# Optimization experiments

Hardware: AMD Instinct MI355X
Metric: run time of the kernel (lower is better)

## Reference

```python
import jax, jax.numpy as jnp
import numpy as np

B, L, C, H, W, R = 2, 16, 64, 64, 128, 32
MH = 32          # forcing MLP hidden
M1, M2 = 8, 8    # spectral conv modes


def _conv2d(x, w, b):
    # x: (N, C, H, W), w: (O, C, kh, kw), SAME padding
    y = jax.lax.conv_general_dilated(x, w, (1, 1), 'SAME',
                                     dimension_numbers=('NCHW', 'OIHW', 'NCHW'))
    return y + b[None, :, None, None]


def setup_inputs():
    k = jax.random.split(jax.random.key(0), 24)
    r_min, r_max = 0.8, 0.99
    u1 = jax.random.uniform(k[0], (C, R))
    u2 = jax.random.uniform(k[1], (C, R))
    nu_log = jnp.log(-0.5 * jnp.log(u1 * (r_max ** 2 - r_min ** 2) + r_min ** 2))
    theta_log = jnp.log(u2 * (2.0 * np.pi))
    s = np.float32(1.0 / np.sqrt(C))
    rn = lambda kk, sh, sc=1.0: np.float32(sc) * jax.random.normal(kk, sh, jnp.float32)
    return {
        'x': rn(k[2], (B, L, C, H, W)),
        'nu_log': nu_log.astype(jnp.float32),
        'theta_log': theta_log.astype(jnp.float32),
        'mlp_w1': rn(k[3], (C, MH), 0.02), 'mlp_b1': jnp.zeros((MH,), jnp.float32),
        'mlp_w2': rn(k[4], (MH, C * R * 2), 0.02), 'mlp_b2': jnp.zeros((C * R * 2,), jnp.float32),
        'forcing_scale': jnp.asarray(0.1, jnp.float32),
        'U_r': rn(k[5], (C, H, R), 1.0 / np.sqrt(H)), 'U_i': rn(k[6], (C, H, R), 1.0 / np.sqrt(H)),
        'V_r': rn(k[7], (C, W, R), 1.0 / np.sqrt(W)), 'V_i': rn(k[8], (C, W, R), 1.0 / np.sqrt(W)),
        'projW_r': rn(k[9], (C, C), s), 'projW_i': rn(k[10], (C, C), s),
        'projb_r': jnp.zeros((C,), jnp.float32), 'projb_i': jnp.zeros((C,), jnp.float32),
        'swr1': rn(k[11], (C, C, M1, M2), s), 'swi1': rn(k[12], (C, C, M1, M2), s),
        'swr2': rn(k[13], (C, C, M1, M2), s), 'swi2': rn(k[14], (C, C, M1, M2), s),
        'convr_w': rn(k[15], (C, C, 3, 3), 0.05), 'convr_b': jnp.zeros((C,), jnp.float32),
        'convi_w': rn(k[16], (C, C, 3, 3), 0.05), 'convi_b': jnp.zeros((C,), jnp.float32),
        'fuse_w': rn(k[17], (C, 2 * C), s), 'fuse_b': jnp.zeros((C,), jnp.float32),
        'gate_w': rn(k[18], (C, C), s), 'gate_b': jnp.zeros((C,), jnp.float32),
        'ln_w': jnp.ones((H, W), jnp.float32), 'ln_b': jnp.zeros((H, W), jnp.float32),
    }


def reference(x, nu_log, theta_log, mlp_w1, mlp_b1, mlp_w2, mlp_b2, forcing_scale,
              U_r, U_i, V_r, V_i, projW_r, projW_i, projb_r, projb_i,
              swr1, swi1, swr2, swi2, convr_w, convr_b, convi_w, convi_b,
              fuse_w, fuse_b, gate_w, gate_b, ln_w, ln_b):
    b_, l_, c_, h_, w_ = x.shape
    # --- selective forcing: spatial-mean context modulates LRU poles ---
    ctx = x.mean((-2, -1))                                       # (B,L,C)
    hmid = jnp.tanh(ctx @ mlp_w1 + mlp_b1)
    delta = (hmid @ mlp_w2 + mlp_b2).reshape(b_, l_, 2, c_, R)
    nu = jnp.exp(nu_log + forcing_scale * delta[:, :, 0])        # (B,L,C,R)
    th = jnp.exp(theta_log + forcing_scale * delta[:, :, 1])
    lam = jnp.exp(1j * th - nu)                                  # |lam| = exp(-nu) in (0,1)
    gamma = jnp.sqrt(1.0 - jnp.exp(-2.0 * nu))                   # input normalization
    # --- spectral encode + low-rank projection ---
    U = U_r + 1j * U_i                                           # (C,H,R)
    V = V_r + 1j * V_i                                           # (C,W,R)
    xf = jnp.fft.fft2(x)                                         # (B,L,C,H,W) complex64
    u = jnp.einsum('blchw,chr,cwr->blcr', xf, U, V)              # rank-R forcing
    # --- time-varying diagonal linear recurrence via parallel scan ---
    def comb(e1, e2):
        a1, b1 = e1
        a2, b2 = e2
        return a2 * a1, a2 * b1 + b2
    _, hstate = jax.lax.associative_scan(
        comb, (lam.astype(u.dtype), gamma.astype(u.dtype) * u), axis=1)
    # --- decode back to frequency grid, channel mix ---
    yf = jnp.einsum('blcr,chr,cwr->blchw', hstate, U, V)
    projW = projW_r + 1j * projW_i
    yf = jnp.einsum('blchw,oc->blohw', yf, projW) \
         + (projb_r + 1j * projb_i)[None, None, :, None, None]
    # --- spectral-conv frequency prior (low modes, both corners) ---
    w1 = swr1 + 1j * swi1
    w2 = swr2 + 1j * swi2
    sp = jnp.zeros_like(xf)
    sp = sp.at[:, :, :, :M1, :M2].set(
        jnp.einsum('blcxy,ocxy->bloxy', xf[:, :, :, :M1, :M2], w1))
    sp = sp.at[:, :, :, -M1:, :M2].set(
        jnp.einsum('blcxy,ocxy->bloxy', xf[:, :, :, -M1:, :M2], w2))
    yf = yf + sp
    # --- back to space, real/imag convs, fusion, LN, gate, residual ---
    y = jnp.fft.ifft2(yf)
    yr = _conv2d(y.real.reshape(b_ * l_, c_, h_, w_), convr_w, convr_b)
    yi = _conv2d(y.imag.reshape(b_ * l_, c_, h_, w_), convi_w, convi_b)
    fused = jnp.concatenate([yr, yi], axis=1).reshape(b_, l_, 2 * c_, h_, w_)
    out = jnp.einsum('blkhw,ok->blohw', fused, fuse_w) \
          + fuse_b[None, None, :, None, None]
    mu = out.mean((-2, -1), keepdims=True)
    var = out.var((-2, -1), keepdims=True)
    out = (out - mu) / jnp.sqrt(var + 1e-5) * ln_w + ln_b
    gate = jax.nn.sigmoid(jnp.einsum('blchw,oc->blohw', x, gate_w)
                          + gate_b[None, None, :, None, None])
    return x + gate * out
```

## Files before the change

### kernel.cpp

```cpp
#include <hip/hip_runtime.h>
#include <math.h>


constexpr int B_ = 2, L_ = 16, C = 64, H = 64, W = 128, R = 32, MH = 32;
constexpr int BL = B_ * L_;
constexpr int HW = H * W;
constexpr int CR = C * R;
constexpr float PI2 = 6.28318530717958647692f;

#define DEV __device__ __forceinline__

typedef __attribute__((ext_vector_type(8))) short bf16x8;
typedef __attribute__((ext_vector_type(4))) float f32x4;

static DEV unsigned short f2bf(float f) {
  unsigned u = __float_as_uint(f);
  u = u + 0x7fffu + ((u >> 16) & 1u);
  return (unsigned short)(u >> 16);
}

__global__ __launch_bounds__(128) void k_trig(float* __restrict__ t64,
                                              float* __restrict__ t128,
                                              unsigned short* __restrict__ Ehat) {
  int i = threadIdx.x;
  if (i < 64) {
    float s, c; sincosf(PI2 * (float)i / 64.0f, &s, &c);
    t64[2 * i] = c; t64[2 * i + 1] = s;
  }
  float s, c; sincosf(PI2 * (float)i / 128.0f, &s, &c);
  t128[2 * i] = c; t128[2 * i + 1] = s;
  for (int j = 0; j < 16; j++) {
    int idx = j * 128 + i;
    int row = idx >> 6, hh = idx & 63;
    int i1 = row & 15, p = row >> 4;
    int m1 = i1 < 8 ? i1 : 48 + i1;
    float ang = PI2 * (float)((m1 * hh) & 63) / 64.0f;
    float s2, c2; sincosf(ang, &s2, &c2);
    Ehat[row * 64 + hh] = f2bf(p ? -s2 : c2);
  }
}

__global__ __launch_bounds__(256) void k_utab(const float* __restrict__ Ur,
                                              const float* __restrict__ Ui,
                                              const float* __restrict__ t64,
                                              float* __restrict__ Uhat,
                                              float* __restrict__ Util) {
  int c = blockIdx.x;
  __shared__ float tt[128];
  if (threadIdx.x < 128) tt[threadIdx.x] = t64[threadIdx.x];
  __syncthreads();
  for (int t = 0; t < 8; t++) {
    int idx = t * 256 + threadIdx.x;
    int hp = idx >> 5, r = idx & 31;
    float fr = 0, fi = 0, br = 0, bi = 0;
    for (int h = 0; h < H; h++) {
      float ur = Ur[(c * H + h) * R + r], ui = Ui[(c * H + h) * R + r];
      int ph = (h * hp) & 63;
      float cs = tt[2 * ph], sn = tt[2 * ph + 1];
      fr += ur * cs + ui * sn;
      fi += ui * cs - ur * sn;
      br += ur * cs - ui * sn;
      bi += ui * cs + ur * sn;
    }
    int o = ((c * H + hp) * R + r) * 2;
    Uhat[o] = fr; Uhat[o + 1] = fi;
    Util[o] = br * (1.0f / H); Util[o + 1] = bi * (1.0f / H);
  }
}

__global__ __launch_bounds__(256) void k_vtab(const float* __restrict__ Vr,
                                              const float* __restrict__ Vi,
                                              const float* __restrict__ t128,
                                              unsigned short* __restrict__ Vhb,
                                              unsigned short* __restrict__ Vt2r,
                                              unsigned short* __restrict__ Vt2i) {
  int c = blockIdx.x;
  __shared__ float tt[256];
  tt[threadIdx.x] = t128[threadIdx.x];
  __syncthreads();
  for (int t = 0; t < 16; t++) {
    int idx = t * 256 + threadIdx.x;
    int wp = idx >> 5, r = idx & 31;
    float fr = 0, fi = 0, br = 0, bi = 0;
    for (int w = 0; w < W; w++) {
      float vr = Vr[(c * W + w) * R + r], vi = Vi[(c * W + w) * R + r];
      int ph = (w * wp) & 127;
      float cs = tt[2 * ph], sn = tt[2 * ph + 1];
      fr += vr * cs + vi * sn;
      fi += vi * cs - vr * sn;
      br += vr * cs - vi * sn;
      bi += vi * cs + vr * sn;
    }
    Vhb[((size_t)c * 64 + 2 * r) * 128 + wp] = f2bf(fr);
    Vhb[((size_t)c * 64 + 2 * r + 1) * 128 + wp] = f2bf(fi);
    Vt2r[(size_t)(c * W + wp) * R + r] = f2bf(br * (1.0f / W));
    Vt2i[(size_t)(c * W + wp) * R + r] = f2bf(bi * (1.0f / W));
  }
}

__global__ __launch_bounds__(256) void k_wb(const float* __restrict__ fuse_w,
                                            const float* __restrict__ convr_w,
                                            const float* __restrict__ convi_w,
                                            unsigned short* __restrict__ Wb) {
  int po = blockIdx.x; int p = po >> 6, o = po & 63;
  const float* cw = p ? convi_w : convr_w;
  __shared__ float fw[64];
  if (threadIdx.x < 64) fw[threadIdx.x] = fuse_w[o * (2 * C) + p * C + threadIdx.x];
  __syncthreads();
  for (int t = 0; t < 3; t++) {
    int idx = t * 256 + threadIdx.x;
    if (idx < 576) {
      int tap = idx >> 6, c = idx & 63;
      float s = 0;
      for (int k = 0; k < C; k++) s += fw[k] * cw[(k * C + c) * 9 + tap];
      Wb[((size_t)(p * 9 + tap) * C + o) * C + c] = f2bf(s);
    }
  }
}

__global__ __launch_bounds__(64) void k_btil(const float* __restrict__ fuse_w,
                                             const float* __restrict__ rb,
                                             const float* __restrict__ ib,
                                             const float* __restrict__ fb,
                                             float* __restrict__ btil) {
  int o = threadIdx.x;
  float s = fb[o];
  for (int k = 0; k < C; k++)
    s += fuse_w[o * (2 * C) + k] * rb[k] + fuse_w[o * (2 * C) + C + k] * ib[k];
  btil[o] = s;
}

__global__ __launch_bounds__(128) void k_p2(const float* __restrict__ pwr,
                                            const float* __restrict__ pwi,
                                            unsigned short* __restrict__ P2) {
  int o = blockIdx.x;
  int k = threadIdx.x;
  int c = k >> 1, odd = k & 1;
  float pr = pwr[o * C + c], pi = pwi[o * C + c];
  float vr = odd ? -pi : pr;
  float vi = odd ? pr : pi;
  int boff = (k * 2) ^ ((o & 7) << 4);
  *(unsigned short*)((char*)P2 + o * 256 + boff) = f2bf(vr);
  *(unsigned short*)((char*)P2 + 16384 + o * 256 + boff) = f2bf(vi);
}

__global__ __launch_bounds__(256) void k_mlp(const float* __restrict__ ctx,
                                             const float* __restrict__ w1,
                                             const float* __restrict__ b1,
                                             const float* __restrict__ w2,
                                             const float* __restrict__ b2,
                                             const float* __restrict__ fs_p,
                                             const float* __restrict__ nu_log,
                                             const float* __restrict__ th_log,
                                             float* __restrict__ lamr,
                                             float* __restrict__ lami,
                                             float* __restrict__ gam) {
  int bl = blockIdx.x;
  __shared__ float cs[C];
  __shared__ float hm[MH];
  if (threadIdx.x < C) cs[threadIdx.x] = ctx[bl * C + threadIdx.x];
  __syncthreads();
  if (threadIdx.x < MH) {
    float s = b1[threadIdx.x];
    for (int k = 0; k < C; k++) s += cs[k] * w1[k * MH + threadIdx.x];
    hm[threadIdx.x] = tanhf(s);
  }
  __syncthreads();
  float fs = fs_p[0];
  for (int t = 0; t < 8; t++) {
    int idx = t * 256 + threadIdx.x;
    float d0 = b2[idx], d1 = b2[CR + idx];
    for (int m = 0; m < MH; m++) {
      float hv = hm[m];
      d0 += hv * w2[m * (2 * CR) + idx];
      d1 += hv * w2[m * (2 * CR) + CR + idx];
    }
    float nu = expf(nu_log[idx] + fs * d0);
    float th = expf(th_log[idx] + fs * d1);
    float en = expf(-nu);
    float sn, cn; sincosf(th, &sn, &cn);
    int o = bl * CR + idx;
    lamr[o] = en * cn; lami[o] = en * sn;
    gam[o] = sqrtf(fmaxf(0.0f, 1.0f - en * en));
  }
}

__global__ __launch_bounds__(256) void k_encode(
    const float* __restrict__ x, const unsigned short* __restrict__ Vhb,
    const float* __restrict__ Uhat, const unsigned short* __restrict__ Ehat,
    const float* __restrict__ t128, float* __restrict__ ub,
    float* __restrict__ Xm, float* __restrict__ ctx) {
  int blc = blockIdx.x;
  int c = blc & 63;
  __shared__ __align__(16) char ldsA[16384];
  __shared__ __align__(16) char ldsB[16384];
  __shared__ float red[4];
  int tid = threadIdx.x;
  int lane = tid & 63;
  int wv = __builtin_amdgcn_readfirstlane(tid >> 6);
  int col = lane & 15, kg = lane >> 4;

  const float4* px4 = (const float4*)(x + (size_t)blc * HW);
  float csum = 0;
  #pragma unroll
  for (int j = 0; j < 8; j++) {
    int e4 = j * 256 + tid;
    float4 v = px4[e4];
    csum += (v.x + v.y) + (v.z + v.w);
    int elem = e4 * 4;
    int h = elem >> 7, w = elem & 127;
    unsigned p0 = (unsigned)f2bf(v.x) | ((unsigned)f2bf(v.y) << 16);
    unsigned p1 = (unsigned)f2bf(v.z) | ((unsigned)f2bf(v.w) << 16);
    int ba = (h * 256 + w * 2) ^ ((h & 7) << 4);
    *(uint2*)(ldsA + ba) = make_uint2(p0, p1);
    unsigned short t0 = f2bf(v.x), t1 = f2bf(v.y), t2 = f2bf(v.z), t3 = f2bf(v.w);
    *(unsigned short*)(ldsB + (((w + 0) * 128 + h * 2) ^ (((w + 0) & 7) << 4))) = t0;
    *(unsigned short*)(ldsB + (((w + 1) * 128 + h * 2) ^ (((w + 1) & 7) << 4))) = t1;
    *(unsigned short*)(ldsB + (((w + 2) * 128 + h * 2) ^ (((w + 2) & 7) << 4))) = t2;
    *(unsigned short*)(ldsB + (((w + 3) * 128 + h * 2) ^ (((w + 3) & 7) << 4))) = t3;
  }
  #pragma unroll
  for (int m = 32; m; m >>= 1) csum += __shfl_xor(csum, m);
  if (lane == 0) red[wv] = csum;
  __syncthreads();
  if (tid == 0)
    ctx[blc] = (red[0] + red[1] + red[2] + red[3]) * (1.0f / HW);

  f32x4 acc1[4];
  #pragma unroll
  for (int nt = 0; nt < 4; nt++) acc1[nt] = (f32x4){0, 0, 0, 0};
  int hA = wv * 16 + col;
  #pragma unroll
  for (int ks = 0; ks < 4; ks++) {
    int k0 = ks * 32 + kg * 8;
    bf16x8 a = *(const bf16x8*)(ldsA + ((hA * 256 + k0 * 2) ^ ((hA & 7) << 4)));
    #pragma unroll
    for (int nt = 0; nt < 4; nt++) {
      int n = nt * 16 + col;
      bf16x8 b = *(const bf16x8*)(Vhb + ((size_t)c * 64 + n) * 128 + k0);
      acc1[nt] = __builtin_amdgcn_mfma_f32_16x16x32_bf16(a, b, acc1[nt], 0, 0, 0);
    }
  }
  f32x4 acc2[2][2];
  #pragma unroll
  for (int mt = 0; mt < 2; mt++)
    for (int nt = 0; nt < 2; nt++) acc2[mt][nt] = (f32x4){0, 0, 0, 0};
  #pragma unroll
  for (int ks = 0; ks < 2; ks++) {
    int k0 = ks * 32 + kg * 8;
    bf16x8 a2[2];
    #pragma unroll
    for (int mt = 0; mt < 2; mt++)
      a2[mt] = *(const bf16x8*)(Ehat + (mt * 16 + col) * 64 + k0);
    #pragma unroll
    for (int nt = 0; nt < 2; nt++) {
      int w = wv * 32 + nt * 16 + col;
      bf16x8 b2 = *(const bf16x8*)(ldsB + ((w * 128 + k0 * 2) ^ ((w & 7) << 4)));
      #pragma unroll
      for (int mt = 0; mt < 2; mt++)
        acc2[mt][nt] = __builtin_amdgcn_mfma_f32_16x16x32_bf16(a2[mt], b2, acc2[mt][nt], 0, 0, 0);
    }
  }
  __syncthreads();
  #pragma unroll
  for (int nt = 0; nt < 4; nt++) {
    int r2 = nt * 16 + col;
    #pragma unroll
    for (int j = 0; j < 4; j++) {
      int h = wv * 16 + kg * 4 + j;
      *(float*)(ldsA + ((h * 256 + r2 * 4) ^ ((h & 7) << 4))) = acc1[nt][j];
    }
  }
  #pragma unroll
  for (int mt = 0; mt < 2; mt++)
    for (int nt = 0; nt < 2; nt++)
      #pragma unroll
      for (int j = 0; j < 4; j++) {
        int mrow = mt * 16 + kg * 4 + j;
        int w = wv * 32 + nt * 16 + col;
        *(float*)(ldsB + ((mrow * 512 + w * 4) ^ ((mrow & 7) << 4))) = acc2[mt][nt][j];
      }
  __syncthreads();

  {
    int r = tid >> 3, hg = tid & 7;
    float ar = 0, ai = 0;
    #pragma unroll
    for (int j = 0; j < 8; j++) {
      int h = hg + 8 * j;
      float2 sv = *(const float2*)(ldsA + ((h * 256 + r * 8) ^ ((h & 7) << 4)));
      const float* up = Uhat + (((size_t)c * H + h) * R + r) * 2;
      float ur = up[0], ui = up[1];
      ar += ur * sv.x - ui * sv.y;
      ai += ur * sv.y + ui * sv.x;
    }
    ar += __shfl_xor(ar, 1); ai += __shfl_xor(ai, 1);
    ar += __shfl_xor(ar, 2); ai += __shfl_xor(ai, 2);
    ar += __shfl_xor(ar, 4); ai += __shfl_xor(ai, 4);
    if (hg == 0) {
      ub[((size_t)blc * R + r) * 2] = ar;
      ub[((size_t)blc * R + r) * 2 + 1] = ai;
    }
  }
  {
    int i1 = tid >> 4, m2 = (tid >> 1) & 7, half = tid & 1;
    float ar = 0, ai = 0;
    for (int jw = 0; jw < 64; jw++) {
      int w = half * 64 + jw;
      float fr = *(const float*)(ldsB + ((i1 * 512 + w * 4) ^ ((i1 & 7) << 4)));
      float fi = *(const float*)(ldsB + (((16 + i1) * 512 + w * 4) ^ ((i1 & 7) << 4)));
      int ph = (m2 * w) & 127;
      float cs = t128[2 * ph], sn = t128[2 * ph + 1];
      ar += fr * cs + fi * sn;
      ai += fi * cs - fr * sn;
    }
    ar += __shfl_xor(ar, 1); ai += __shfl_xor(ai, 1);
    if (half == 0) {
      Xm[((size_t)blc * 128 + i1 * 8 + m2) * 2] = ar;
      Xm[((size_t)blc * 128 + i1 * 8 + m2) * 2 + 1] = ai;
    }
  }
}

__global__ __launch_bounds__(256) void k_scan(const float* __restrict__ lamr,
                                              const float* __restrict__ lami,
                                              const float* __restrict__ gam,
                                              const float* __restrict__ ub,
                                              float* __restrict__ hs) {
  int idx = blockIdx.x * 256 + threadIdx.x;
  int b = idx >> 11, cr = idx & 2047;
  float hr = 0, hi = 0;
  for (int l = 0; l < L_; l++) {
    int o = (b * L_ + l) * CR + cr;
    float lr = lamr[o], li = lami[o], g = gam[o];
    float ur = ub[2 * o], ui = ub[2 * o + 1];
    float nr = lr * hr - li * hi + g * ur;
    float ni = lr * hi + li * hr + g * ui;
    hr = nr; hi = ni;
    hs[2 * o] = hr; hs[2 * o + 1] = hi;
  }
}

__global__ __launch_bounds__(256) void k_spm(const float* __restrict__ Xm,
                                             const float* __restrict__ w1r,
                                             const float* __restrict__ w1i,
                                             const float* __restrict__ w2r,
                                             const float* __restrict__ w2i,
                                             float* __restrict__ SPm) {
  int bl = blockIdx.x;
  int o0 = blockIdx.y * 8;
  const float* px = Xm + (size_t)bl * C * 256;
  for (int t = 0; t < 4; t++) {
    int idx = t * 256 + threadIdx.x;
    int o = o0 + (idx >> 7), mode = idx & 127;
    int i1 = mode >> 3, m2 = mode & 7;
    const float* wr; const float* wi; int ii;
    if (i1 < 8) { wr = w1r; wi = w1i; ii = i1; }
    else        { wr = w2r; wi = w2i; ii = i1 - 8; }
    float ar = 0, ai = 0;
    for (int cc = 0; cc < C; cc++) {
      float xr = px[(cc * 128 + mode) * 2], xi = px[(cc * 128 + mode) * 2 + 1];
      float wrr = wr[((size_t)(o * C + cc) * 8 + ii) * 8 + m2];
      float wii = wi[((size_t)(o * C + cc) * 8 + ii) * 8 + m2];
      ar += xr * wrr - xi * wii;
      ai += xr * wii + xi * wrr;
    }
    size_t oo = (size_t)bl * C * 128 + (size_t)o * 128 + mode;
    SPm[oo * 2] = ar * (1.0f / HW);
    SPm[oo * 2 + 1] = ai * (1.0f / HW);
  }
}

__global__ __launch_bounds__(256) void k_q(const float* __restrict__ SPm,
                                           const float* __restrict__ t64,
                                           float* __restrict__ Qb) {
  int blo = blockIdx.x;
  __shared__ float sp[256];
  int tid = threadIdx.x;
  sp[tid] = SPm[(size_t)blo * 256 + tid];
  __syncthreads();
  for (int t = 0; t < 2; t++) {
    int idx = t * 256 + tid;
    int h = idx >> 3, m2 = idx & 7;
    float ar = 0, ai = 0;
    #pragma unroll
    for (int i1 = 0; i1 < 16; i1++) {
      int m1 = i1 < 8 ? i1 : 48 + i1;
      int ph = (m1 * h) & 63;
      float cs = t64[2 * ph], sn = t64[2 * ph + 1];
      float sr = sp[(i1 * 8 + m2) * 2], si = sp[(i1 * 8 + m2) * 2 + 1];
      ar += sr * cs - si * sn;
      ai += sr * sn + si * cs;
    }
    Qb[((size_t)blo * H * 8 + idx) * 2] = ar;
    Qb[((size_t)blo * H * 8 + idx) * 2 + 1] = ai;
  }
}

__global__ __launch_bounds__(256) void k_y(
    const float* __restrict__ hs, const float* __restrict__ Util,
    const unsigned short* __restrict__ Vt2r,
    const unsigned short* __restrict__ Vt2i,
    unsigned* __restrict__ y2) {
  int bl = blockIdx.x;
  int h0 = blockIdx.y * 16;
  int zz = blockIdx.z;
  int w0 = (zz >> 4) * 64;
  int chunk = zz & 15;
  int tid = threadIdx.x;
  int lane = tid & 63;
  int wv = __builtin_amdgcn_readfirstlane(tid >> 6);
  __shared__ unsigned ybuf[1024 * 4];
  int row = lane & 15;
  int kg = lane >> 4;
  int c = chunk * 4 + wv;
  const float* up = Util + (((size_t)c * H + h0 + row) * R + kg * 8) * 2;
  const float* hp = hs + (((size_t)bl * C + c) * R + kg * 8) * 2;
  bf16x8 aGr, aGi, aGn;
  #pragma unroll
  for (int j = 0; j < 8; j++) {
    float ur = up[2 * j], ui = up[2 * j + 1];
    float hr = hp[2 * j], hi = hp[2 * j + 1];
    float gr = hr * ur - hi * ui, gi = hr * ui + hi * ur;
    aGr[j] = (short)f2bf(gr); aGi[j] = (short)f2bf(gi);
    aGn[j] = (short)f2bf(-gi);
  }
  #pragma unroll
  for (int nt = 0; nt < 4; nt++) {
    int w = w0 + nt * 16 + row;
    const unsigned short* vr = Vt2r + ((size_t)c * W + w) * R + kg * 8;
    const unsigned short* vi = Vt2i + ((size_t)c * W + w) * R + kg * 8;
    bf16x8 bVr = *(const bf16x8*)vr;
    bf16x8 bVi = *(const bf16x8*)vi;
    f32x4 accr = {0, 0, 0, 0}, acci = {0, 0, 0, 0};
    accr = __builtin_amdgcn_mfma_f32_16x16x32_bf16(aGr, bVr, accr, 0, 0, 0);
    accr = __builtin_amdgcn_mfma_f32_16x16x32_bf16(aGn, bVi, accr, 0, 0, 0);
    acci = __builtin_amdgcn_mfma_f32_16x16x32_bf16(aGr, bVi, acci, 0, 0, 0);
    acci = __builtin_amdgcn_mfma_f32_16x16x32_bf16(aGi, bVr, acci, 0, 0, 0);
    #pragma unroll
    for (int r = 0; r < 4; r++) {
      int hl = kg * 4 + r;
      unsigned pk = (unsigned)f2bf(accr[r]) | ((unsigned)f2bf(acci[r]) << 16);
      ybuf[(hl * 64 + nt * 16 + row) * 4 + wv] = pk;
    }
  }
  __syncthreads();
  #pragma unroll
  for (int q = 0; q < 4; q++) {
    int p = q * 256 + tid;
    int lh = p >> 6, lw = p & 63;
    uint4 v = *(const uint4*)&ybuf[p * 4];
    size_t pixg = ((size_t)bl * H + h0 + lh) * W + (w0 + lw);
    int off = (chunk * 16) ^ ((lw & 7) << 4);
    *(uint4*)((char*)y2 + pixg * 256 + off) = v;
  }
}

__global__ __launch_bounds__(256) void k_proj(
    const unsigned* __restrict__ y2, const unsigned short* __restrict__ P2,
    const float* __restrict__ Qb, const float* __restrict__ pbr,
    const float* __restrict__ pbi, const float* __restrict__ t128,
    unsigned short* __restrict__ Zr, unsigned short* __restrict__ Zi) {
  int bl = blockIdx.x;
  int h = blockIdx.y;
  int tid = threadIdx.x, lane = tid & 63;
  int wv = __builtin_amdgcn_readfirstlane(tid >> 6);
  __shared__ __align__(16) char ylds[32768];
  __shared__ __align__(16) char plds[32768];
  {
    const uint4* gy = (const uint4*)((const char*)y2 +
                                     ((size_t)bl * H + h) * W * 256);
    const uint4* gp = (const uint4*)P2;
    uint4* ly = (uint4*)ylds; uint4* lp = (uint4*)plds;
    for (int i = tid; i < 2048; i += 256) ly[i] = gy[i];
    for (int i = tid; i < 2048; i += 256) lp[i] = gp[i];
  }
  __syncthreads();
  int col = lane & 15, kg = lane >> 4;
  f32x4 zr[4][2], zi[4][2];
  #pragma unroll
  for (int mt = 0; mt < 4; mt++)
    for (int nt = 0; nt < 2; nt++) { zr[mt][nt] = (f32x4){0,0,0,0}; zi[mt][nt] = (f32x4){0,0,0,0}; }
  #pragma unroll
  for (int ks = 0; ks < 4; ks++) {
    int koff = ks * 64 + kg * 16;
    bf16x8 ar[4], ai[4];
    #pragma unroll
    for (int mt = 0; mt < 4; mt++) {
      int o = mt * 16 + col;
      int ab = o * 256 + (koff ^ ((o & 7) << 4));
      ar[mt] = *(const bf16x8*)(plds + ab);
      ai[mt] = *(const bf16x8*)(plds + 16384 + ab);
    }
    #pragma unroll
    for (int nt = 0; nt < 2; nt++) {
      int pix = wv * 32 + nt * 16 + col;
      bf16x8 b = *(const bf16x8*)(ylds + pix * 256 + (koff ^ ((pix & 7) << 4)));
      #pragma unroll
      for (int mt = 0; mt < 4; mt++) {
        zr[mt][nt] = __builtin_amdgcn_mfma_f32_16x16x32_bf16(ar[mt], b, zr[mt][nt], 0, 0, 0);
        zi[mt][nt] = __builtin_amdgcn_mfma_f32_16x16x32_bf16(ai[mt], b, zi[mt][nt], 0, 0, 0);
      }
    }
  }
  #pragma unroll
  for (int nt = 0; nt < 2; nt++) {
    int w = wv * 32 + nt * 16 + col;
    float csv[8], snv[8];
    #pragma unroll
    for (int m2 = 0; m2 < 8; m2++) {
      int ph = (m2 * w) & 127;
      csv[m2] = t128[2 * ph]; snv[m2] = t128[2 * ph + 1];
    }
    #pragma unroll
    for (int mt = 0; mt < 4; mt++) {
      float vrr[4], vii[4];
      #pragma unroll
      for (int r = 0; r < 4; r++) {
        int o = mt * 16 + kg * 4 + r;
        const float* qp = Qb + ((size_t)(bl * C + o) * H + h) * 16;
        float vr = zr[mt][nt][r], vi = zi[mt][nt][r];
        #pragma unroll
        for (int m2 = 0; m2 < 8; m2++) {
          float qr = qp[2 * m2], qi = qp[2 * m2 + 1];
          vr += qr * csv[m2] - qi * snv[m2];
          vi += qr * snv[m2] + qi * csv[m2];
        }
        if (h == 0 && w == 0) { vr += pbr[o]; vi += pbi[o]; }
        vrr[r] = vr; vii[r] = vi;
      }
      size_t zoff = (((size_t)bl * H + h) * W + w) * C + mt * 16 + kg * 4;
      unsigned p0 = f2bf(vrr[0]) | ((unsigned)f2bf(vrr[1]) << 16);
      unsigned p1 = f2bf(vrr[2]) | ((unsigned)f2bf(vrr[3]) << 16);
      *(uint2*)(Zr + zoff) = make_uint2(p0, p1);
      unsigned q0 = f2bf(vii[0]) | ((unsigned)f2bf(vii[1]) << 16);
      unsigned q1 = f2bf(vii[2]) | ((unsigned)f2bf(vii[3]) << 16);
      *(uint2*)(Zi + zoff) = make_uint2(q0, q1);
    }
  }
}

__global__ __launch_bounds__(256) void k_conv(const unsigned short* __restrict__ Zr,
                                              const unsigned short* __restrict__ Zi,
                                              const unsigned short* __restrict__ Wb,
                                              const float* __restrict__ btil,
                                              float* __restrict__ outp) {
  int bl = blockIdx.x >> 6;
  int h = blockIdx.x & 63;
  int tid = threadIdx.x;
  int lane = tid & 63;
  int wv = __builtin_amdgcn_readfirstlane(tid >> 6);
  __shared__ __align__(16) char zs[130 * 128];
  f32x4 acc[4][2];
  #pragma unroll
  for (int mt = 0; mt < 4; mt++)
    for (int nt = 0; nt < 2; nt++) acc[mt][nt] = (f32x4){0, 0, 0, 0};

  for (int p = 0; p < 2; p++) {
    const unsigned short* Z = p ? Zi : Zr;
    for (int dh = 0; dh < 3; dh++) {
      int hr = h + dh - 1;
      __syncthreads();
      if (hr >= 0 && hr < H) {
        const uint4* src = (const uint4*)(Z + ((size_t)(bl * H + hr)) * W * C);
        #pragma unroll
        for (int i = 0; i < 4; i++) {
          int ch = tid * 4 + i;
          int ws = 1 + (ch >> 3), c2 = (ch & 7) * 16;
          int byte = (ws * 128 + c2) ^ ((ws & 7) << 4);
          *(uint4*)(zs + byte) = src[ch];
        }
      } else {
        #pragma unroll
        for (int i = 0; i < 4; i++) {
          int ch = tid * 4 + i;
          int ws = 1 + (ch >> 3), c2 = (ch & 7) * 16;
          int byte = (ws * 128 + c2) ^ ((ws & 7) << 4);
          *(uint4*)(zs + byte) = make_uint4(0, 0, 0, 0);
        }
      }
      if (tid < 16) {
        int ws = (tid < 8) ? 0 : 129; int c2 = (tid & 7) * 16;
        int byte = (ws * 128 + c2) ^ ((ws & 7) << 4);
        *(uint4*)(zs + byte) = make_uint4(0, 0, 0, 0);
      }
      __syncthreads();
      #pragma unroll
      for (int kc = 0; kc < 2; kc++) {
        #pragma unroll
        for (int dw = 0; dw < 3; dw++) {
          int tap = dh * 3 + dw;
          bf16x8 bfr[2];
          #pragma unroll
          for (int nt = 0; nt < 2; nt++) {
            int ws = wv * 32 + nt * 16 + (lane & 15) + dw;
            int byte = (ws * 128 + (kc * 32 + (lane >> 4) * 8) * 2) ^ ((ws & 7) << 4);
            bfr[nt] = *(const bf16x8*)(zs + byte);
          }
          const unsigned short* wbp =
              Wb + ((size_t)(p * 9 + tap) * C) * C + kc * 32 + (lane >> 4) * 8;
          #pragma unroll
          for (int mt = 0; mt < 4; mt++) {
            bf16x8 af = *(const bf16x8*)(wbp + (size_t)(mt * 16 + (lane & 15)) * C);
            acc[mt][0] = __builtin_amdgcn_mfma_f32_16x16x32_bf16(af, bfr[0], acc[mt][0], 0, 0, 0);
            acc[mt][1] = __builtin_amdgcn_mfma_f32_16x16x32_bf16(af, bfr[1], acc[mt][1], 0, 0, 0);
          }
        }
      }
    }
  }
  #pragma unroll
  for (int mt = 0; mt < 4; mt++) {
    #pragma unroll
    for (int nt = 0; nt < 2; nt++) {
      int w = wv * 32 + nt * 16 + (lane & 15);
      #pragma unroll
      for (int r = 0; r < 4; r++) {
        int o = mt * 16 + (lane >> 4) * 4 + r;
        outp[((size_t)(bl * C + o) * H + h) * W + w] = acc[mt][nt][r] + btil[o];
      }
    }
  }
}

__global__ __launch_bounds__(256) void k_lnstats(const float* __restrict__ outp,
                                                 float* __restrict__ mu,
                                                 float* __restrict__ rstd) {
  int i = blockIdx.x;
  const float4* p = (const float4*)(outp + (size_t)i * HW);
  float s = 0, q = 0;
  for (int t = threadIdx.x; t < HW / 4; t += 256) {
    float4 v = p[t];
    s += (v.x + v.y) + (v.z + v.w);
    q += (v.x * v.x + v.y * v.y) + (v.z * v.z + v.w * v.w);
  }
  #pragma unroll
  for (int o2 = 32; o2; o2 >>= 1) { s += __shfl_down(s, o2); q += __shfl_down(q, o2); }
  __shared__ float rs[4], rq[4];
  if ((threadIdx.x & 63) == 0) { rs[threadIdx.x >> 6] = s; rq[threadIdx.x >> 6] = q; }
  __syncthreads();
  if (threadIdx.x == 0) {
    float S = rs[0] + rs[1] + rs[2] + rs[3];
    float Q = rq[0] + rq[1] + rq[2] + rq[3];
    float m = S * (1.0f / HW);
    float var = Q * (1.0f / HW) - m * m;
    mu[i] = m; rstd[i] = rsqrtf(var + 1e-5f);
  }
}

__global__ __launch_bounds__(256) void k_final(const float* __restrict__ x,
                                               const float* __restrict__ gw,
                                               const float* __restrict__ gb,
                                               const float* __restrict__ mu,
                                               const float* __restrict__ rstd,
                                               const float* __restrict__ lnw,
                                               const float* __restrict__ lnb,
                                               float* __restrict__ outp) {
  int bl = blockIdx.x >> 6, h = blockIdx.x & 63;
  int tid = threadIdx.x;
  __shared__ float xs[C * W];
  for (int i = tid; i < C * W; i += 256) {
    int c = i >> 7, w = i & 127;
    xs[i] = x[((size_t)(bl * C + c) * H + h) * W + w];
  }
  __syncthreads();
  int w = tid & 127;
  int oh = __builtin_amdgcn_readfirstlane(tid >> 7);
  float glin[32];
  #pragma unroll
  for (int i = 0; i < 32; i++) glin[i] = gb[oh * 32 + i];
  for (int cc = 0; cc < C; cc++) {
    float xv = xs[cc * W + w];
    const float* gwp = gw + (size_t)(oh * 32) * C + cc;
    #pragma unroll
    for (int i = 0; i < 32; i++) glin[i] += gwp[(size_t)i * C] * xv;
  }
  float lw = lnw[h * W + w], lb = lnb[h * W + w];
  #pragma unroll
  for (int i = 0; i < 32; i++) {
    int o = oh * 32 + i;
    size_t off = ((size_t)(bl * C + o) * H + h) * W + w;
    float m = mu[bl * C + o], rs = rstd[bl * C + o];
    float op = outp[off];
    float nrm = (op - m) * rs * lw + lb;
    float sg = 1.0f / (1.0f + expf(-glin[i]));
    outp[off] = xs[o * W + w] + sg * nrm;
  }
}

extern "C" void kernel_launch(void* const* d_in, const int* in_sizes, int n_in,
                              void* d_out, int out_size, void* d_ws,
                              size_t ws_size, hipStream_t stream) {
  const float* x       = (const float*)d_in[0];
  const float* nu_log  = (const float*)d_in[1];
  const float* th_log  = (const float*)d_in[2];
  const float* mlp_w1  = (const float*)d_in[3];
  const float* mlp_b1  = (const float*)d_in[4];
  const float* mlp_w2  = (const float*)d_in[5];
  const float* mlp_b2  = (const float*)d_in[6];
  const float* fscale  = (const float*)d_in[7];
  const float* U_r     = (const float*)d_in[8];
  const float* U_i     = (const float*)d_in[9];
  const float* V_r     = (const float*)d_in[10];
  const float* V_i     = (const float*)d_in[11];
  const float* pW_r    = (const float*)d_in[12];
  const float* pW_i    = (const float*)d_in[13];
  const float* pb_r    = (const float*)d_in[14];
  const float* pb_i    = (const float*)d_in[15];
  const float* swr1    = (const float*)d_in[16];
  const float* swi1    = (const float*)d_in[17];
  const float* swr2    = (const float*)d_in[18];
  const float* swi2    = (const float*)d_in[19];
  const float* convr_w = (const float*)d_in[20];
  const float* convr_b = (const float*)d_in[21];
  const float* convi_w = (const float*)d_in[22];
  const float* convi_b = (const float*)d_in[23];
  const float* fuse_w  = (const float*)d_in[24];
  const float* fuse_b  = (const float*)d_in[25];
  const float* gate_w  = (const float*)d_in[26];
  const float* gate_b  = (const float*)d_in[27];
  const float* ln_w    = (const float*)d_in[28];
  const float* ln_b    = (const float*)d_in[29];
  float* outp = (float*)d_out;

  char* wsb = (char*)d_ws;
  size_t off = 0;
  auto alloc = [&](size_t nbytes) -> void* {
    void* p = (void*)(wsb + off);
    off += ((nbytes + 255) / 256) * 256;
    return p;
  };
  float* trig64  = (float*)alloc(128 * 4);
  float* trig128 = (float*)alloc(256 * 4);
  unsigned short* Ehat = (unsigned short*)alloc(32 * 64 * 2);
  float* Uhat = (float*)alloc((size_t)C * H * R * 2 * 4);
  float* Util = (float*)alloc((size_t)C * H * R * 2 * 4);
  unsigned short* Vhb = (unsigned short*)alloc((size_t)C * 64 * 128 * 2);
  unsigned short* Vt2r = (unsigned short*)alloc((size_t)C * W * R * 2);
  unsigned short* Vt2i = (unsigned short*)alloc((size_t)C * W * R * 2);
  unsigned short* Wb = (unsigned short*)alloc((size_t)2 * 9 * C * C * 2);
  float* btil = (float*)alloc(C * 4);
  unsigned short* P2 = (unsigned short*)alloc((size_t)2 * C * 128 * 2);
  float* ctx  = (float*)alloc(BL * C * 4);
  float* lamr = (float*)alloc(BL * CR * 4);
  float* lami = (float*)alloc(BL * CR * 4);
  float* gam  = (float*)alloc(BL * CR * 4);
  float* ub   = (float*)alloc((size_t)BL * CR * 2 * 4);
  float* hs   = (float*)alloc((size_t)BL * CR * 2 * 4);
  float* Xm   = (float*)alloc((size_t)BL * C * 128 * 2 * 4);
  float* SPm  = (float*)alloc((size_t)BL * C * 128 * 2 * 4);
  float* Qb   = (float*)alloc((size_t)BL * C * H * 8 * 2 * 4);
  unsigned* y2 = (unsigned*)alloc((size_t)BL * HW * C * 4);
  unsigned short* Zr = (unsigned short*)alloc((size_t)BL * HW * C * 2);
  unsigned short* Zi = (unsigned short*)alloc((size_t)BL * HW * C * 2);
  float* mu   = (float*)alloc(BL * C * 4);
  float* rstd = (float*)alloc(BL * C * 4);

  k_trig<<<1, 128, 0, stream>>>(trig64, trig128, Ehat);
  k_utab<<<C, 256, 0, stream>>>(U_r, U_i, trig64, Uhat, Util);
  k_vtab<<<C, 256, 0, stream>>>(V_r, V_i, trig128, Vhb, Vt2r, Vt2i);
  k_wb<<<2 * C, 256, 0, stream>>>(fuse_w, convr_w, convi_w, Wb);
  k_btil<<<1, 64, 0, stream>>>(fuse_w, convr_b, convi_b, fuse_b, btil);
  k_p2<<<C, 128, 0, stream>>>(pW_r, pW_i, P2);
  k_encode<<<BL * C, 256, 0, stream>>>(x, Vhb, Uhat, Ehat, trig128, ub, Xm, ctx);
  k_mlp<<<BL, 256, 0, stream>>>(ctx, mlp_w1, mlp_b1, mlp_w2, mlp_b2, fscale,
                                nu_log, th_log, lamr, lami, gam);
  k_scan<<<16, 256, 0, stream>>>(lamr, lami, gam, ub, hs);
  k_spm<<<dim3(BL, 8), 256, 0, stream>>>(Xm, swr1, swi1, swr2, swi2, SPm);
  k_q<<<BL * C, 256, 0, stream>>>(SPm, trig64, Qb);
  k_y<<<dim3(BL, 4, 32), 256, 0, stream>>>(hs, Util, Vt2r, Vt2i, y2);
  k_proj<<<dim3(BL, H), 256, 0, stream>>>(y2, P2, Qb, pb_r, pb_i, trig128,
                                          Zr, Zi);
  k_conv<<<BL * H, 256, 0, stream>>>(Zr, Zi, Wb, btil, outp);
  k_lnstats<<<BL * C, 256, 0, stream>>>(outp, mu, rstd);
  k_final<<<BL * H, 256, 0, stream>>>(x, gate_w, gate_b, mu, rstd, ln_w, ln_b,
                                      outp);
}
```

Measured before the change: 881.2 us.

## Double-buffer conv row staging and make y2 layout chunk-major for coalescing

The conv kernel now double-buffers its LDS row tile. It prefetches the next input row into registers while MFMAs consume the current buffer, which cuts one barrier per step and hides global load latency. Separately, the y2 intermediate changes from a per-pixel swizzled 256-byte layout to a chunk-major layout. The swizzle is now applied when k_proj writes into LDS. This is meant to make stores and loads coalesce better, but it doubles LDS for the conv and uses more registers for the prefetch.

New measurement: 851.9 us. 3.3% less time.

```diff
diff --git a/kernel.cpp b/kernel.cpp
--- a/kernel.cpp
+++ b/kernel.cpp
@@ -451,8 +451,7 @@
     int lh = p >> 6, lw = p & 63;
     uint4 v = *(const uint4*)&ybuf[p * 4];
     size_t pixg = ((size_t)bl * H + h0 + lh) * W + (w0 + lw);
-    int off = (chunk * 16) ^ ((lw & 7) << 4);
-    *(uint4*)((char*)y2 + pixg * 256 + off) = v;
+    *(uint4*)((char*)y2 + ((size_t)chunk * BL * HW + pixg) * 16) = v;
   }
 }
 
@@ -468,11 +467,18 @@
   __shared__ __align__(16) char ylds[32768];
   __shared__ __align__(16) char plds[32768];
   {
-    const uint4* gy = (const uint4*)((const char*)y2 +
-                                     ((size_t)bl * H + h) * W * 256);
+    const char* gyb = (const char*)y2;
+    #pragma unroll
+    for (int k2 = 0; k2 < 8; k2++) {
+      int idx = k2 * 256 + tid;
+      int chunk = idx >> 7, w = idx & 127;
+      uint4 v = *(const uint4*)(gyb +
+          ((size_t)chunk * BL * HW + (size_t)bl * HW + h * W + w) * 16);
+      int byte = (w * 256 + chunk * 16) ^ ((w & 7) << 4);
+      *(uint4*)(ylds + byte) = v;
+    }
     const uint4* gp = (const uint4*)P2;
-    uint4* ly = (uint4*)ylds; uint4* lp = (uint4*)plds;
-    for (int i = tid; i < 2048; i += 256) ly[i] = gy[i];
+    uint4* lp = (uint4*)plds;
     for (int i = tid; i < 2048; i += 256) lp[i] = gp[i];
   }
   __syncthreads();
@@ -550,64 +556,74 @@
   int tid = threadIdx.x;
   int lane = tid & 63;
   int wv = __builtin_amdgcn_readfirstlane(tid >> 6);
-  __shared__ __align__(16) char zs[130 * 128];
+  __shared__ __align__(16) char zs[2][130 * 128];
   f32x4 acc[4][2];
   #pragma unroll
   for (int mt = 0; mt < 4; mt++)
     for (int nt = 0; nt < 2; nt++) acc[mt][nt] = (f32x4){0, 0, 0, 0};
 
-  for (int p = 0; p < 2; p++) {
-    const unsigned short* Z = p ? Zi : Zr;
-    for (int dh = 0; dh < 3; dh++) {
-      int hr = h + dh - 1;
-      __syncthreads();
-      if (hr >= 0 && hr < H) {
-        const uint4* src = (const uint4*)(Z + ((size_t)(bl * H + hr)) * W * C);
+  if (tid < 32) {
+    int b = tid >> 4, hws = (tid >> 3) & 1, cch = tid & 7;
+    int ws = hws ? 129 : 0;
+    int byte = (ws * 128 + cch * 16) ^ ((ws & 7) << 4);
+    *(uint4*)(zs[b] + byte) = make_uint4(0, 0, 0, 0);
+  }
+
+  auto ldrow = [&](int s, uint4* v) {
+    int p = s >= 3 ? 1 : 0, dh = s - p * 3;
+    int hr = h + dh - 1;
+    if (hr >= 0 && hr < H) {
+      const uint4* src = (const uint4*)((p ? Zi : Zr) +
+                                        ((size_t)(bl * H + hr)) * W * C);
+      #pragma unroll
+      for (int i = 0; i < 4; i++) v[i] = src[i * 256 + tid];
+    } else {
+      #pragma unroll
+      for (int i = 0; i < 4; i++) v[i] = make_uint4(0, 0, 0, 0);
+    }
+  };
+  auto wrrow = [&](char* buf, const uint4* v) {
+    #pragma unroll
+    for (int i = 0; i < 4; i++) {
+      int ch = i * 256 + tid;
+      int ws = 1 + (ch >> 3), c2 = (ch & 7) * 16;
+      int byte = (ws * 128 + c2) ^ ((ws & 7) << 4);
+      *(uint4*)(buf + byte) = v[i];
+    }
+  };
+
+  uint4 v[4];
+  ldrow(0, v);
+  wrrow(zs[0], v);
+  #pragma unroll
+  for (int s = 0; s < 6; s++) {
+    int cur = s & 1;
+    if (s < 5) ldrow(s + 1, v);
+    __syncthreads();
+    int p = s >= 3 ? 1 : 0, dh = s - p * 3;
+    #pragma unroll
+    for (int kc = 0; kc < 2; kc++) {
+      #pragma unroll
+      for (int dw = 0; dw < 3; dw++) {
+        int tap = dh * 3 + dw;
+        bf16x8 bfr[2];
         #pragma unroll
-        for (int i = 0; i < 4; i++) {
-          int ch = tid * 4 + i;
-          int ws = 1 + (ch >> 3), c2 = (ch & 7) * 16;
-          int byte = (ws * 128 + c2) ^ ((ws & 7) << 4);
-          *(uint4*)(zs + byte) = src[ch];
+        for (int nt = 0; nt < 2; nt++) {
+          int ws = wv * 32 + nt * 16 + (lane & 15) + dw;
+          int byte = (ws * 128 + (kc * 32 + (lane >> 4) * 8) * 2) ^ ((ws & 7) << 4);
+          bfr[nt] = *(const bf16x8*)(zs[cur] + byte);
         }
-      } else {
+        const unsigned short* wbp =
+            Wb + ((size_t)(p * 9 + tap) * C) * C + kc * 32 + (lane >> 4) * 8;
         #pragma unroll
-        for (int i = 0; i < 4; i++) {
-          int ch = tid * 4 + i;
-          int ws = 1 + (ch >> 3), c2 = (ch & 7) * 16;
-          int byte = (ws * 128 + c2) ^ ((ws & 7) << 4);
-          *(uint4*)(zs + byte) = make_uint4(0, 0, 0, 0);
+        for (int mt = 0; mt < 4; mt++) {
+          bf16x8 af = *(const bf16x8*)(wbp + (size_t)(mt * 16 + (lane & 15)) * C);
+          acc[mt][0] = __builtin_amdgcn_mfma_f32_16x16x32_bf16(af, bfr[0], acc[mt][0], 0, 0, 0);
+          acc[mt][1] = __builtin_amdgcn_mfma_f32_16x16x32_bf16(af, bfr[1], acc[mt][1], 0, 0, 0);
         }
       }
-      if (tid < 16) {
-        int ws = (tid < 8) ? 0 : 129; int c2 = (tid & 7) * 16;
-        int byte = (ws * 128 + c2) ^ ((ws & 7) << 4);
-        *(uint4*)(zs + byte) = make_uint4(0, 0, 0, 0);
-      }
-      __syncthreads();
-      #pragma unroll
-      for (int kc = 0; kc < 2; kc++) {
-        #pragma unroll
-        for (int dw = 0; dw < 3; dw++) {
-          int tap = dh * 3 + dw;
-          bf16x8 bfr[2];
-          #pragma unroll
-          for (int nt = 0; nt < 2; nt++) {
-            int ws = wv * 32 + nt * 16 + (lane & 15) + dw;
-            int byte = (ws * 128 + (kc * 32 + (lane >> 4) * 8) * 2) ^ ((ws & 7) << 4);
-            bfr[nt] = *(const bf16x8*)(zs + byte);
-          }
-          const unsigned short* wbp =
-              Wb + ((size_t)(p * 9 + tap) * C) * C + kc * 32 + (lane >> 4) * 8;
-          #pragma unroll
-          for (int mt = 0; mt < 4; mt++) {
-            bf16x8 af = *(const bf16x8*)(wbp + (size_t)(mt * 16 + (lane & 15)) * C);
-            acc[mt][0] = __builtin_amdgcn_mfma_f32_16x16x32_bf16(af, bfr[0], acc[mt][0], 0, 0, 0);
-            acc[mt][1] = __builtin_amdgcn_mfma_f32_16x16x32_bf16(af, bfr[1], acc[mt][1], 0, 0, 0);
-          }
-        }
-      }
-    }
+    }
+    if (s < 5) wrrow(zs[cur ^ 1], v);
   }
   #pragma unroll
   for (int mt = 0; mt < 4; mt++) {
```
